# Performance work log

Hardware: AMD Instinct MI355X
Metric: run time of the kernel (lower is better)

The kernel has to match this reference:

```python
import jax, jax.numpy as jnp
import numpy as np
import itertools

G = 80          # voxel grid side
N = 200000      # active voxels
A, B = 64, 128  # in/out channels
K = 27          # 3x3x3 kernel offsets
EPS = 1e-5


def _build_kernel_map():
    rng = np.random.default_rng(0)
    flat = rng.choice(G ** 3, size=N, replace=False)
    coords = np.stack(np.unravel_index(flat, (G, G, G)), axis=1).astype(np.int64)  # [N,3]
    lookup = np.full(G ** 3, -1, dtype=np.int64)
    lookup[flat] = np.arange(N)
    gidx = np.full((K, N), N, dtype=np.int32)  # pad with dummy row N
    sidx = np.full((K, N), N, dtype=np.int32)
    for k, off in enumerate(itertools.product([-1, 0, 1], repeat=3)):
        nb = coords + np.asarray(off)
        valid = np.all((nb >= 0) & (nb < G), axis=1)
        i_all = np.nonzero(valid)[0]
        nbf = np.ravel_multi_index(nb[valid].T, (G, G, G))
        j = lookup[nbf]
        m = j >= 0
        i, j = i_all[m], j[m]
        e = len(i)
        gidx[k, :e] = j   # gather neighbor features
        sidx[k, :e] = i   # scatter to output voxel
    return jnp.asarray(gidx), jnp.asarray(sidx)


def setup_inputs() -> dict:
    key = jax.random.key(0)
    ks = jax.random.split(key, 8)
    gidx, sidx = _build_kernel_map()
    return {
        "feats": jax.random.normal(ks[0], (N, A), jnp.float32),
        "w1": jax.random.normal(ks[1], (K, A, B), jnp.float32) * (1.0 / np.sqrt(K * A)),
        "w2": jax.random.normal(ks[2], (K, B, B), jnp.float32) * (1.0 / np.sqrt(K * B)),
        "w_nin": jax.random.normal(ks[3], (A, B), jnp.float32) * (1.0 / np.sqrt(A)),
        "bn1_gamma": jnp.ones((A,), jnp.float32),
        "bn1_beta": jnp.zeros((A,), jnp.float32),
        "bn2_gamma": jnp.ones((B,), jnp.float32),
        "bn2_beta": jnp.zeros((B,), jnp.float32),
        "gidx": gidx,
        "sidx": sidx,
    }


def _bn(x, gamma, beta):
    # MinkowskiBatchNorm: per-channel stats over all active voxels (training mode)
    mean = jnp.mean(x, axis=0)
    var = jnp.var(x, axis=0)
    return (x - mean) * jax.lax.rsqrt(var + EPS) * gamma + beta


def _sparse_conv(feats, w, gidx, sidx):
    # Minkowski sparse conv: for each kernel offset k, gather neighbor feats,
    # apply W[k], scatter-add to output voxel. Dummy row N absorbs padding.
    fp = jnp.concatenate([feats, jnp.zeros((1, feats.shape[1]), feats.dtype)], axis=0)
    out = jnp.zeros((N + 1, w.shape[-1]), feats.dtype)
    for k in range(w.shape[0]):  # fixed 27 offsets
        out = out.at[sidx[k]].add(fp[gidx[k]] @ w[k])
    return out[:N]


def reference(feats, w1, w2, w_nin, bn1_gamma, bn1_beta, bn2_gamma, bn2_beta, gidx, sidx):
    # resblock: BN(a) -> conv3(a->b) -> BN(b) -> conv3(b->b); skip via 1x1 conv (a!=b)
    h = _bn(feats, bn1_gamma, bn1_beta)
    h = _sparse_conv(h, w1, gidx, sidx)
    h = _bn(h, bn2_gamma, bn2_beta)
    residual = _sparse_conv(h, w2, gidx, sidx)
    skip = feats @ w_nin  # kernel_size=1 conv == per-voxel linear
    return skip + residual
```

## Files before the change

### kernel.cpp

```cpp
#include <hip/hip_runtime.h>

#define N_VOX 200000
#define NPAD_INV (27 * N_VOX + 128)
#define EPS_BN 1e-5f

typedef __bf16 bf16x8 __attribute__((ext_vector_type(8)));
typedef float f32x4 __attribute__((ext_vector_type(4)));

__device__ __forceinline__ float bf2f(unsigned short u) {
    union { float f; unsigned int i; } x; x.i = ((unsigned int)u) << 16; return x.f;
}
__device__ __forceinline__ unsigned short f2bf(float f) {
    union { float f; unsigned int i; } x; x.f = f;
    unsigned int r = x.i + 0x7fffu + ((x.i >> 16) & 1u);
    return (unsigned short)(r >> 16);
}

#define ASYNC16(gsrc, ldst)                                                             \
    __builtin_amdgcn_global_load_lds(                                                   \
        (const __attribute__((address_space(1))) void*)(gsrc),                          \
        (__attribute__((address_space(3))) void*)(ldst), 16, 0, 0)

__global__ void fill_inv_kernel(int* __restrict__ inv) {
    for (int i = blockIdx.x * 256 + threadIdx.x; i < NPAD_INV; i += gridDim.x * 256)
        inv[i] = N_VOX;
}

__global__ void build_inv_kernel(const int* __restrict__ sidx, const int* __restrict__ gidx,
                                 int* __restrict__ inv) {
    int k = blockIdx.y;
    int p = blockIdx.x * 256 + threadIdx.x;
    if (p < N_VOX) {
        int s = sidx[k * N_VOX + p];
        if (s < N_VOX) inv[k * N_VOX + s] = gidx[k * N_VOX + p];
    }
}

__global__ void tr_w1_kernel(const float* __restrict__ w, unsigned short* __restrict__ wt) {
    int k = blockIdx.y; int idx = blockIdx.x * 256 + threadIdx.x;
    int a = idx >> 7, b = idx & 127;
    wt[k * 8192 + b * 64 + a] = f2bf(w[k * 8192 + idx]);
}
__global__ void tr_w2_kernel(const float* __restrict__ w, unsigned short* __restrict__ wt) {
    int k = blockIdx.y; int idx = blockIdx.x * 256 + threadIdx.x;
    int a = idx >> 7, b = idx & 127;
    wt[k * 16384 + b * 128 + a] = f2bf(w[k * 16384 + idx]);
}
__global__ void tr_wn_kernel(const float* __restrict__ w, unsigned short* __restrict__ wt) {
    int idx = blockIdx.x * 256 + threadIdx.x;
    int a = idx >> 7, b = idx & 127;
    wt[b * 64 + a] = f2bf(w[idx]);
}

__global__ void stats1_kernel(const float* __restrict__ feats,
                              float* __restrict__ sum, float* __restrict__ sq) {
    int t = threadIdx.x; int c = t & 63; int rg = t >> 6;
    float s = 0.f, q = 0.f;
    for (int row = blockIdx.x * 4 + rg; row < N_VOX; row += gridDim.x * 4) {
        float x = feats[(size_t)row * 64 + c];
        s += x; q += x * x;
    }
    __shared__ float red[8][64];
    red[rg][c] = s; red[4 + rg][c] = q;
    __syncthreads();
    if (t < 64) atomicAdd(&sum[t], red[0][t] + red[1][t] + red[2][t] + red[3][t]);
    else if (t < 128) { int cc = t - 64; atomicAdd(&sq[cc], red[4][cc] + red[5][cc] + red[6][cc] + red[7][cc]); }
}

__global__ void stats2_kernel(const unsigned short* __restrict__ h1b,
                              float* __restrict__ sum, float* __restrict__ sq) {
    int t = threadIdx.x; int c = t & 127; int rg = t >> 7;
    float s = 0.f, q = 0.f;
    for (int row = blockIdx.x * 2 + rg; row < N_VOX; row += gridDim.x * 2) {
        float x = bf2f(h1b[(size_t)row * 128 + c]);
        s += x; q += x * x;
    }
    __shared__ float red[4][128];
    red[rg][c] = s; red[2 + rg][c] = q;
    __syncthreads();
    if (t < 128) atomicAdd(&sum[t], red[0][t] + red[1][t]);
    else { int cc = t - 128; atomicAdd(&sq[cc], red[2][cc] + red[3][cc]); }
}

__global__ void norm1_kernel(const float* __restrict__ feats, const float* __restrict__ ssum,
                             const float* __restrict__ ssq, const float* __restrict__ gamma,
                             const float* __restrict__ beta, unsigned short* __restrict__ fA,
                             unsigned short* __restrict__ fRaw) {
    __shared__ float sc[64], sh[64];
    int t = threadIdx.x;
    if (t < 64) {
        float mean = ssum[t] * (1.0f / N_VOX);
        float var  = ssq[t] * (1.0f / N_VOX) - mean * mean;
        float s    = gamma[t] * rsqrtf(var + EPS_BN);
        sc[t] = s; sh[t] = beta[t] - mean * s;
    }
    __syncthreads();
    const int total = N_VOX * 64 / 8;
    int i = blockIdx.x * 256 + t;
    if (i >= total) return;
    int cb = (i * 8) & 63;
    const float4* src = (const float4*)(feats + (size_t)i * 8);
    float4 f0 = src[0], f1 = src[1];
    float fv[8] = {f0.x, f0.y, f0.z, f0.w, f1.x, f1.y, f1.z, f1.w};
    union { uint4 q; unsigned short u[8]; } a, r;
#pragma unroll
    for (int j = 0; j < 8; j++) {
        a.u[j] = f2bf(fv[j] * sc[cb + j] + sh[cb + j]);
        r.u[j] = f2bf(fv[j]);
    }
    *(uint4*)(fA + (size_t)i * 8) = a.q;
    *(uint4*)(fRaw + (size_t)i * 8) = r.q;
}

__global__ void norm2_kernel(unsigned short* __restrict__ h1b, const float* __restrict__ ssum,
                             const float* __restrict__ ssq, const float* __restrict__ gamma,
                             const float* __restrict__ beta) {
    __shared__ float sc[128], sh[128];
    int t = threadIdx.x;
    if (t < 128) {
        float mean = ssum[t] * (1.0f / N_VOX);
        float var  = ssq[t] * (1.0f / N_VOX) - mean * mean;
        float s    = gamma[t] * rsqrtf(var + EPS_BN);
        sc[t] = s; sh[t] = beta[t] - mean * s;
    }
    __syncthreads();
    const int total = N_VOX * 128 / 8;
    int i = blockIdx.x * 256 + t;
    if (i >= total) return;
    int cb = (i * 8) & 127;
    union { uint4 q; unsigned short u[8]; } v;
    v.q = *(const uint4*)(h1b + (size_t)i * 8);
#pragma unroll
    for (int j = 0; j < 8; j++) v.u[j] = f2bf(bf2f(v.u[j]) * sc[cb + j] + sh[cb + j]);
    *(uint4*)(h1b + (size_t)i * 8) = v.q;
}

__global__ __launch_bounds__(256) void conv1_kernel(
    const unsigned short* __restrict__ fA, const unsigned short* __restrict__ w1t,
    const int* __restrict__ inv, const unsigned short* __restrict__ zp,
    unsigned short* __restrict__ h1b) {
    __shared__ __align__(16) unsigned short sA[128 * 64];
    __shared__ __align__(16) unsigned short sB[128 * 64];
    const int t = threadIdx.x, lane = t & 63, w = t >> 6;
    const int v0 = blockIdx.x * 128;
    const int srow = w * 32;
    const int lrow = lane >> 3;
    const int lcol = (lane & 7) * 8;
    const int m0 = (w & 1) * 64, n0 = (w >> 1) * 64;
    const int l16 = lane & 15, quad = lane >> 4;
    f32x4 acc[4][4] = {};

    for (int k = 0; k < 27; k++) {
#pragma unroll
        for (int q = 0; q < 4; q++) {
            int rt = srow + q * 8 + lrow;
            int g = inv[k * N_VOX + v0 + rt];
            const unsigned short* asrc = (g < N_VOX) ? (fA + (size_t)g * 64 + lcol) : (zp + lcol);
            ASYNC16(asrc, &sA[(srow + q * 8) * 64]);
            const unsigned short* bsrc = w1t + k * 8192 + rt * 64 + lcol;
            ASYNC16(bsrc, &sB[(srow + q * 8) * 64]);
        }
        __syncthreads();
#pragma unroll
        for (int ks = 0; ks < 2; ks++) {
            bf16x8 af[4], bfr[4];
#pragma unroll
            for (int mi = 0; mi < 4; mi++)
                af[mi] = *(const bf16x8*)&sA[(m0 + mi * 16 + l16) * 64 + ks * 32 + quad * 8];
#pragma unroll
            for (int ni = 0; ni < 4; ni++)
                bfr[ni] = *(const bf16x8*)&sB[(n0 + ni * 16 + l16) * 64 + ks * 32 + quad * 8];
#pragma unroll
            for (int mi = 0; mi < 4; mi++)
#pragma unroll
                for (int ni = 0; ni < 4; ni++)
                    acc[mi][ni] = __builtin_amdgcn_mfma_f32_16x16x32_bf16(af[mi], bfr[ni], acc[mi][ni], 0, 0, 0);
        }
        __syncthreads();
    }
#pragma unroll
    for (int mi = 0; mi < 4; mi++)
#pragma unroll
        for (int r = 0; r < 4; r++) {
            int v = v0 + m0 + mi * 16 + quad * 4 + r;
            if (v < N_VOX) {
#pragma unroll
                for (int ni = 0; ni < 4; ni++)
                    h1b[(size_t)v * 128 + n0 + ni * 16 + l16] = f2bf(acc[mi][ni][r]);
            }
        }
}

__global__ __launch_bounds__(256) void conv2_kernel(
    const unsigned short* __restrict__ h1n, const unsigned short* __restrict__ fRaw,
    const unsigned short* __restrict__ w2t, const unsigned short* __restrict__ w_nint,
    const int* __restrict__ inv, const unsigned short* __restrict__ zp,
    float* __restrict__ out) {
    __shared__ __align__(16) unsigned short sA[128 * 64];
    __shared__ __align__(16) unsigned short sB[128 * 64];
    const int t = threadIdx.x, lane = t & 63, w = t >> 6;
    const int v0 = blockIdx.x * 128;
    const int srow = w * 32;
    const int lrow = lane >> 3;
    const int lcol = (lane & 7) * 8;
    const int m0 = (w & 1) * 64, n0 = (w >> 1) * 64;
    const int l16 = lane & 15, quad = lane >> 4;
    f32x4 acc[4][4] = {};

    for (int jj = 0; jj < 55; jj++) {
        if (jj < 54) {
            const int ko = jj >> 1;
            const int kh = (jj & 1) * 64;
#pragma unroll
            for (int q = 0; q < 4; q++) {
                int rt = srow + q * 8 + lrow;
                int g = inv[ko * N_VOX + v0 + rt];
                const unsigned short* asrc = (g < N_VOX) ? (h1n + (size_t)g * 128 + kh + lcol) : (zp + lcol);
                ASYNC16(asrc, &sA[(srow + q * 8) * 64]);
                const unsigned short* bsrc = w2t + ko * 16384 + rt * 128 + kh + lcol;
                ASYNC16(bsrc, &sB[(srow + q * 8) * 64]);
            }
        } else {
#pragma unroll
            for (int q = 0; q < 4; q++) {
                int rt = srow + q * 8 + lrow;
                int v = v0 + rt;
                const unsigned short* asrc = (v < N_VOX) ? (fRaw + (size_t)v * 64 + lcol) : (zp + lcol);
                ASYNC16(asrc, &sA[(srow + q * 8) * 64]);
                const unsigned short* bsrc = w_nint + rt * 64 + lcol;
                ASYNC16(bsrc, &sB[(srow + q * 8) * 64]);
            }
        }
        __syncthreads();
#pragma unroll
        for (int ks = 0; ks < 2; ks++) {
            bf16x8 af[4], bfr[4];
#pragma unroll
            for (int mi = 0; mi < 4; mi++)
                af[mi] = *(const bf16x8*)&sA[(m0 + mi * 16 + l16) * 64 + ks * 32 + quad * 8];
#pragma unroll
            for (int ni = 0; ni < 4; ni++)
                bfr[ni] = *(const bf16x8*)&sB[(n0 + ni * 16 + l16) * 64 + ks * 32 + quad * 8];
#pragma unroll
            for (int mi = 0; mi < 4; mi++)
#pragma unroll
                for (int ni = 0; ni < 4; ni++)
                    acc[mi][ni] = __builtin_amdgcn_mfma_f32_16x16x32_bf16(af[mi], bfr[ni], acc[mi][ni], 0, 0, 0);
        }
        __syncthreads();
    }
#pragma unroll
    for (int mi = 0; mi < 4; mi++)
#pragma unroll
        for (int r = 0; r < 4; r++) {
            int v = v0 + m0 + mi * 16 + quad * 4 + r;
            if (v < N_VOX) {
#pragma unroll
                for (int ni = 0; ni < 4; ni++)
                    out[(size_t)v * 128 + n0 + ni * 16 + l16] = acc[mi][ni][r];
            }
        }
}

extern "C" void kernel_launch(void* const* d_in, const int* in_sizes, int n_in,
                              void* d_out, int out_size, void* d_ws, size_t ws_size,
                              hipStream_t stream) {
    const float* feats = (const float*)d_in[0];
    const float* w1    = (const float*)d_in[1];
    const float* w2    = (const float*)d_in[2];
    const float* w_nin = (const float*)d_in[3];
    const float* g1    = (const float*)d_in[4];
    const float* b1    = (const float*)d_in[5];
    const float* g2    = (const float*)d_in[6];
    const float* b2    = (const float*)d_in[7];
    const int* gidx = (const int*)d_in[8];
    const int* sidx = (const int*)d_in[9];
    float* out = (float*)d_out;

    char* ws = (char*)d_ws;
    int* inv               = (int*)(ws);
    unsigned short* fA     = (unsigned short*)(ws + 21600512);
    unsigned short* fRaw   = (unsigned short*)(ws + 47200512);
    unsigned short* h1b    = (unsigned short*)(ws + 72800512);
    unsigned short* w1t    = (unsigned short*)(ws + 124000512);
    unsigned short* w2t    = (unsigned short*)(ws + 124442880);
    unsigned short* w_nint = (unsigned short*)(ws + 125327616);
    float* stats           = (float*)(ws + 125344000);
    unsigned short* zp     = (unsigned short*)(ws + 125345536);
    float* s1sum = stats, *s1sq = stats + 64, *s2sum = stats + 128, *s2sq = stats + 256;

    hipMemsetAsync(stats, 0, 1536 + 256, stream);
    fill_inv_kernel<<<2048, 256, 0, stream>>>(inv);
    build_inv_kernel<<<dim3(782, 27), 256, 0, stream>>>(sidx, gidx, inv);
    tr_w1_kernel<<<dim3(32, 27), 256, 0, stream>>>(w1, w1t);
    tr_w2_kernel<<<dim3(64, 27), 256, 0, stream>>>(w2, w2t);
    tr_wn_kernel<<<32, 256, 0, stream>>>(w_nin, w_nint);
    stats1_kernel<<<512, 256, 0, stream>>>(feats, s1sum, s1sq);
    norm1_kernel<<<6250, 256, 0, stream>>>(feats, s1sum, s1sq, g1, b1, fA, fRaw);
    conv1_kernel<<<1563, 256, 0, stream>>>(fA, w1t, inv, zp, h1b);
    stats2_kernel<<<512, 256, 0, stream>>>(h1b, s2sum, s2sq);
    norm2_kernel<<<12500, 256, 0, stream>>>(h1b, s2sum, s2sq, g2, b2);
    conv2_kernel<<<1563, 256, 0, stream>>>(h1b, fRaw, w2t, w_nint, inv, zp, out);
}
```

Measured before the change: 860.0 us.

## Register-prefetch next gather tile and pad LDS rows in sparse conv kernels

Both conv kernels replace direct global-to-LDS async loads with register staging. Each iteration writes the prefetched tile to LDS, then issues the next offset's gather loads into registers before running the MFMAs, so global latency can overlap compute. LDS rows are padded from 64 to 72 elements to avoid bank conflicts on fragment reads. The cost is extra VGPRs for the staging buffers (possibly lower occupancy) and one redundant prefetch on the last iteration.

```diff
diff --git a/kernel.cpp b/kernel.cpp
--- a/kernel.cpp
+++ b/kernel.cpp
@@ -15,11 +15,6 @@
     unsigned int r = x.i + 0x7fffu + ((x.i >> 16) & 1u);
     return (unsigned short)(r >> 16);
 }
-
-#define ASYNC16(gsrc, ldst)                                                             \
-    __builtin_amdgcn_global_load_lds(                                                   \
-        (const __attribute__((address_space(1))) void*)(gsrc),                          \
-        (__attribute__((address_space(3))) void*)(ldst), 16, 0, 0)
 
 __global__ void fill_inv_kernel(int* __restrict__ inv) {
     for (int i = blockIdx.x * 256 + threadIdx.x; i < NPAD_INV; i += gridDim.x * 256)
@@ -139,44 +134,55 @@
     const unsigned short* __restrict__ fA, const unsigned short* __restrict__ w1t,
     const int* __restrict__ inv, const unsigned short* __restrict__ zp,
     unsigned short* __restrict__ h1b) {
-    __shared__ __align__(16) unsigned short sA[128 * 64];
-    __shared__ __align__(16) unsigned short sB[128 * 64];
+    __shared__ __align__(16) unsigned short sA[128 * 72];
+    __shared__ __align__(16) unsigned short sB[128 * 72];
     const int t = threadIdx.x, lane = t & 63, w = t >> 6;
     const int v0 = blockIdx.x * 128;
-    const int srow = w * 32;
-    const int lrow = lane >> 3;
-    const int lcol = (lane & 7) * 8;
+    const int row = t >> 1;
+    const int half = (t & 1) * 32;
     const int m0 = (w & 1) * 64, n0 = (w >> 1) * 64;
     const int l16 = lane & 15, quad = lane >> 4;
     f32x4 acc[4][4] = {};
-
+    uint4 ra[4], rb[4];
+
+    {
+        int g = inv[v0 + row];
+        const uint4* asrc = (const uint4*)((g < N_VOX) ? (fA + (size_t)g * 64 + half) : (zp + half));
+        const uint4* bsrc = (const uint4*)(w1t + row * 64 + half);
+#pragma unroll
+        for (int i = 0; i < 4; i++) { ra[i] = asrc[i]; rb[i] = bsrc[i]; }
+    }
     for (int k = 0; k < 27; k++) {
-#pragma unroll
-        for (int q = 0; q < 4; q++) {
-            int rt = srow + q * 8 + lrow;
-            int g = inv[k * N_VOX + v0 + rt];
-            const unsigned short* asrc = (g < N_VOX) ? (fA + (size_t)g * 64 + lcol) : (zp + lcol);
-            ASYNC16(asrc, &sA[(srow + q * 8) * 64]);
-            const unsigned short* bsrc = w1t + k * 8192 + rt * 64 + lcol;
-            ASYNC16(bsrc, &sB[(srow + q * 8) * 64]);
-        }
         __syncthreads();
+#pragma unroll
+        for (int i = 0; i < 4; i++) {
+            *(uint4*)&sA[row * 72 + half + i * 8] = ra[i];
+            *(uint4*)&sB[row * 72 + half + i * 8] = rb[i];
+        }
+        __syncthreads();
+        {
+            int kn = (k + 1 < 27) ? k + 1 : 0;
+            int g = inv[kn * N_VOX + v0 + row];
+            const uint4* asrc = (const uint4*)((g < N_VOX) ? (fA + (size_t)g * 64 + half) : (zp + half));
+            const uint4* bsrc = (const uint4*)(w1t + kn * 8192 + row * 64 + half);
+#pragma unroll
+            for (int i = 0; i < 4; i++) { ra[i] = asrc[i]; rb[i] = bsrc[i]; }
+        }
 #pragma unroll
         for (int ks = 0; ks < 2; ks++) {
             bf16x8 af[4], bfr[4];
 #pragma unroll
             for (int mi = 0; mi < 4; mi++)
-                af[mi] = *(const bf16x8*)&sA[(m0 + mi * 16 + l16) * 64 + ks * 32 + quad * 8];
+                af[mi] = *(const bf16x8*)&sA[(m0 + mi * 16 + l16) * 72 + ks * 32 + quad * 8];
 #pragma unroll
             for (int ni = 0; ni < 4; ni++)
-                bfr[ni] = *(const bf16x8*)&sB[(n0 + ni * 16 + l16) * 64 + ks * 32 + quad * 8];
+                bfr[ni] = *(const bf16x8*)&sB[(n0 + ni * 16 + l16) * 72 + ks * 32 + quad * 8];
 #pragma unroll
             for (int mi = 0; mi < 4; mi++)
 #pragma unroll
                 for (int ni = 0; ni < 4; ni++)
                     acc[mi][ni] = __builtin_amdgcn_mfma_f32_16x16x32_bf16(af[mi], bfr[ni], acc[mi][ni], 0, 0, 0);
         }
-        __syncthreads();
     }
 #pragma unroll
     for (int mi = 0; mi < 4; mi++)
@@ -196,58 +202,64 @@
     const unsigned short* __restrict__ w2t, const unsigned short* __restrict__ w_nint,
     const int* __restrict__ inv, const unsigned short* __restrict__ zp,
     float* __restrict__ out) {
-    __shared__ __align__(16) unsigned short sA[128 * 64];
-    __shared__ __align__(16) unsigned short sB[128 * 64];
+    __shared__ __align__(16) unsigned short sA[128 * 72];
+    __shared__ __align__(16) unsigned short sB[128 * 72];
     const int t = threadIdx.x, lane = t & 63, w = t >> 6;
     const int v0 = blockIdx.x * 128;
-    const int srow = w * 32;
-    const int lrow = lane >> 3;
-    const int lcol = (lane & 7) * 8;
+    const int row = t >> 1;
+    const int half = (t & 1) * 32;
     const int m0 = (w & 1) * 64, n0 = (w >> 1) * 64;
     const int l16 = lane & 15, quad = lane >> 4;
     f32x4 acc[4][4] = {};
-
+    uint4 ra[4], rb[4];
+
+    {
+        int g = inv[v0 + row];
+        const uint4* asrc = (const uint4*)((g < N_VOX) ? (h1n + (size_t)g * 128 + half) : (zp + half));
+        const uint4* bsrc = (const uint4*)(w2t + row * 128 + half);
+#pragma unroll
+        for (int i = 0; i < 4; i++) { ra[i] = asrc[i]; rb[i] = bsrc[i]; }
+    }
     for (int jj = 0; jj < 55; jj++) {
-        if (jj < 54) {
-            const int ko = jj >> 1;
-            const int kh = (jj & 1) * 64;
-#pragma unroll
-            for (int q = 0; q < 4; q++) {
-                int rt = srow + q * 8 + lrow;
-                int g = inv[ko * N_VOX + v0 + rt];
-                const unsigned short* asrc = (g < N_VOX) ? (h1n + (size_t)g * 128 + kh + lcol) : (zp + lcol);
-                ASYNC16(asrc, &sA[(srow + q * 8) * 64]);
-                const unsigned short* bsrc = w2t + ko * 16384 + rt * 128 + kh + lcol;
-                ASYNC16(bsrc, &sB[(srow + q * 8) * 64]);
+        __syncthreads();
+#pragma unroll
+        for (int i = 0; i < 4; i++) {
+            *(uint4*)&sA[row * 72 + half + i * 8] = ra[i];
+            *(uint4*)&sB[row * 72 + half + i * 8] = rb[i];
+        }
+        __syncthreads();
+        {
+            int jn = (jj + 1 < 55) ? jj + 1 : 0;
+            const uint4* asrc;
+            const uint4* bsrc;
+            if (jn < 54) {
+                int ko = jn >> 1, kh = (jn & 1) * 64;
+                int g = inv[ko * N_VOX + v0 + row];
+                asrc = (const uint4*)((g < N_VOX) ? (h1n + (size_t)g * 128 + kh + half) : (zp + half));
+                bsrc = (const uint4*)(w2t + ko * 16384 + row * 128 + kh + half);
+            } else {
+                int v = v0 + row;
+                asrc = (const uint4*)((v < N_VOX) ? (fRaw + (size_t)v * 64 + half) : (zp + half));
+                bsrc = (const uint4*)(w_nint + row * 64 + half);
             }
-        } else {
-#pragma unroll
-            for (int q = 0; q < 4; q++) {
-                int rt = srow + q * 8 + lrow;
-                int v = v0 + rt;
-                const unsigned short* asrc = (v < N_VOX) ? (fRaw + (size_t)v * 64 + lcol) : (zp + lcol);
-                ASYNC16(asrc, &sA[(srow + q * 8) * 64]);
-                const unsigned short* bsrc = w_nint + rt * 64 + lcol;
-                ASYNC16(bsrc, &sB[(srow + q * 8) * 64]);
-            }
-        }
-        __syncthreads();
+#pragma unroll
+            for (int i = 0; i < 4; i++) { ra[i] = asrc[i]; rb[i] = bsrc[i]; }
+        }
 #pragma unroll
         for (int ks = 0; ks < 2; ks++) {
             bf16x8 af[4], bfr[4];
 #pragma unroll
             for (int mi = 0; mi < 4; mi++)
-                af[mi] = *(const bf16x8*)&sA[(m0 + mi * 16 + l16) * 64 + ks * 32 + quad * 8];
+                af[mi] = *(const bf16x8*)&sA[(m0 + mi * 16 + l16) * 72 + ks * 32 + quad * 8];
 #pragma unroll
             for (int ni = 0; ni < 4; ni++)
-                bfr[ni] = *(const bf16x8*)&sB[(n0 + ni * 16 + l16) * 64 + ks * 32 + quad * 8];
+                bfr[ni] = *(const bf16x8*)&sB[(n0 + ni * 16 + l16) * 72 + ks * 32 + quad * 8];
 #pragma unroll
             for (int mi = 0; mi < 4; mi++)
 #pragma unroll
                 for (int ni = 0; ni < 4; ni++)
                     acc[mi][ni] = __builtin_amdgcn_mfma_f32_16x16x32_bf16(af[mi], bfr[ni], acc[mi][ni], 0, 0, 0);
         }
-        __syncthreads();
     }
 #pragma unroll
     for (int mi = 0; mi < 4; mi++)
```

Result: slower. 1.602 ms (+86.3%).
